# Kernel tuning notes

Measured on AMD Instinct MI355X. Metric: run time of the kernel, lower is better.

The kernel has to match this reference:

```python
import jax, jax.numpy as jnp
import numpy as np

D_MODEL = 1024
D_STATE = 16
BATCH = 2
SEQ = 2048


def setup_inputs() -> dict:
    key = jax.random.key(0)
    k1, k2, k3, k4, k5 = jax.random.split(key, 5)
    x = jax.random.normal(k1, (BATCH, SEQ, D_MODEL), dtype=jnp.float32)
    log_A_diag = jax.random.normal(k2, (D_MODEL, D_STATE), dtype=jnp.float32)
    B_w = jax.random.normal(k3, (D_STATE, D_MODEL), dtype=jnp.float32) / np.sqrt(D_MODEL)
    C_w = jax.random.normal(k4, (D_MODEL, D_STATE), dtype=jnp.float32) / np.sqrt(D_STATE)
    D_vec = jax.random.normal(k5, (D_MODEL,), dtype=jnp.float32)
    return {"x": x, "log_A_diag": log_A_diag, "B_w": B_w, "C_w": C_w, "D_vec": D_vec}


def reference(x, log_A_diag, B_w, C_w, D_vec):
    # x: (B, L, D)
    B, L, D = x.shape
    pad = 2 * L
    A_bar = jnp.exp(-jnp.exp(log_A_diag))          # (D, S), in (0, 1)
    B_t = jnp.einsum('bld,sd->bls', x, B_w)        # B projection: (B, L, S)
    k_idx = jnp.arange(L, dtype=x.dtype)
    kernel = A_bar[..., None] ** k_idx             # (D, S, L) exponential kernel
    # zero-padded FFT convolution along time axis
    kernel_fft = jnp.fft.rfft(kernel, n=pad, axis=-1)                 # (D, S, L+1)
    B_fft = jnp.fft.rfft(B_t.transpose(0, 2, 1), n=pad, axis=-1)      # (B, S, L+1)
    conv_fft = kernel_fft[None] * B_fft[:, None]                      # (B, D, S, L+1)
    conv = jnp.fft.irfft(conv_fft, n=pad, axis=-1)[..., :L]           # (B, D, S, L)
    # C projection fused over state dim; equivalent to permute->einsum('blds,ds->bld')
    y = jnp.einsum('bdsl,ds->bld', conv, C_w)
    y = y + D_vec[None, None, :] * x               # skip connection
    return y  # dropout is identity in eval mode
```

## Files before the change

### kernel.cpp

```cpp
#include <hip/hip_runtime.h>

#define D_MODEL 1024
#define D_STATE 16
#define BATCH   2
#define SEQ     2048
#define CHUNK   32
#define NCHUNK  (SEQ / CHUNK)
#define NGRP    (SEQ / 4)
#define Q       8
#define SBLEN   (SEQ / Q)
#define SBGRP   (SBLEN / 4)
#define SBCHK   (SBLEN / CHUNK)

__global__ __launch_bounds__(256) void k_bt(const float* __restrict__ x,
                                            const float* __restrict__ Bw,
                                            float* __restrict__ bt,
                                            float* __restrict__ btg) {
    const int t    = threadIdx.x;
    const int wave = t >> 6;
    const int lane = t & 63;

    float4 bw[4][4];
    const float* bwp = Bw + (wave * 4) * D_MODEL + lane * 16;
#pragma unroll
    for (int i = 0; i < 4; ++i)
#pragma unroll
        for (int k = 0; k < 4; ++k)
            bw[i][k] = *(const float4*)(bwp + i * D_MODEL + k * 4);

    const int ROWS = (BATCH * SEQ) / gridDim.x;
    const int row0 = blockIdx.x * ROWS;
    for (int r = 0; r < ROWS; ++r) {
        const int row = row0 + r;
        const float* xr = x + (size_t)row * D_MODEL + lane * 16;
        float4 xv[4];
#pragma unroll
        for (int k = 0; k < 4; ++k) xv[k] = *(const float4*)(xr + k * 4);

        float acc[4] = {0.f, 0.f, 0.f, 0.f};
#pragma unroll
        for (int i = 0; i < 4; ++i) {
#pragma unroll
            for (int k = 0; k < 4; ++k) {
                acc[i] += xv[k].x * bw[i][k].x;
                acc[i] += xv[k].y * bw[i][k].y;
                acc[i] += xv[k].z * bw[i][k].z;
                acc[i] += xv[k].w * bw[i][k].w;
            }
        }
#pragma unroll
        for (int m = 1; m < 64; m <<= 1) {
#pragma unroll
            for (int i = 0; i < 4; ++i) acc[i] += __shfl_xor(acc[i], m, 64);
        }
        if (lane == 0) {
            *(float4*)(bt + (size_t)row * D_STATE + wave * 4) =
                make_float4(acc[0], acc[1], acc[2], acc[3]);
            const int b = row >> 11;
            const int l = row & (SEQ - 1);
            float* p = btg + (((size_t)(b * NGRP + (l >> 2)) * D_STATE + wave * 4) << 2) + (l & 3);
#pragma unroll
            for (int i = 0; i < 4; ++i) p[i * 4] = acc[i];
        }
    }
}

__global__ __launch_bounds__(256) void k_scan_local(const float* __restrict__ btg,
                                                    const float* __restrict__ logA,
                                                    float* __restrict__ carry,
                                                    float* __restrict__ F) {
    const int blk = blockIdx.x;
    const int dt  = blk & 63;
    const int q   = (blk >> 6) & 7;
    const int b   = blk >> 9;
    const int t   = threadIdx.x;
    const int s   = t & 15;
    const int dl  = t >> 4;
    const int d   = dt * 16 + dl;

    __shared__ float sb[SBLEN * D_STATE];
    {
        const float4* src = (const float4*)(btg + (size_t)(b * NGRP + q * SBGRP) * (D_STATE * 4));
        float4* dst = (float4*)sb;
#pragma unroll
        for (int i = 0; i < 4; ++i) dst[t + i * 256] = src[t + i * 256];
    }
    __syncthreads();

    const float A  = expf(-expf(logA[d * D_STATE + s]));
    const float A2 = A * A, A4 = A2 * A2;

    const float4* sb4 = (const float4*)sb;
    float h = 0.f;
    size_t ci = ((size_t)(b * NCHUNK + q * SBCHK) * D_MODEL + d) * D_STATE + s;
#pragma unroll
    for (int k = 0; k < SBCHK; ++k) {
        carry[ci] = h;
        ci += (size_t)D_MODEL * D_STATE;
#pragma unroll
        for (int gg = 0; gg < CHUNK / 4; ++gg) {
            const float4 v = sb4[(k * (CHUNK / 4) + gg) * D_STATE + s];
            h = h * A4 + (((v.x * A + v.y) * A + v.z) * A + v.w);
        }
    }
    F[((size_t)(b * Q + q) * D_MODEL + d) * D_STATE + s] = h;
}

__global__ __launch_bounds__(256) void k_final(const float* __restrict__ x,
                                               const float* __restrict__ logA,
                                               const float* __restrict__ Cw,
                                               const float* __restrict__ Dv,
                                               const float* __restrict__ bt,
                                               const float* __restrict__ carry,
                                               const float* __restrict__ F,
                                               float* __restrict__ y) {
    const int blk = blockIdx.x;
    const int dt  = blk & 3;
    const int c   = (blk >> 2) & (NCHUNK - 1);
    const int b   = blk >> 8;
    const int t   = threadIdx.x;
    const int d   = dt * 256 + t;
    const int q   = c >> 3;
    const int kk  = c & 7;

    float A[D_STATE], C[D_STATE], h[D_STATE];
    const float* lp = logA + (size_t)d * D_STATE;
    const float* cp = Cw + (size_t)d * D_STATE;
    const float* hp = carry + ((size_t)(b * NCHUNK + c) * D_MODEL + d) * D_STATE;
#pragma unroll
    for (int s = 0; s < D_STATE; ++s) {
        A[s] = expf(-expf(lp[s]));
        C[s] = cp[s];
        h[s] = hp[s];
    }

    if (q > 0) {
        float A32[D_STATE], H[D_STATE];
#pragma unroll
        for (int s = 0; s < D_STATE; ++s) {
            float a = A[s];
            a *= a; a *= a; a *= a; a *= a; a *= a;
            A32[s] = a;
            H[s] = 0.f;
        }
        for (int p = 0; p < q; ++p) {
            const float* fp = F + ((size_t)(b * Q + p) * D_MODEL + d) * D_STATE;
#pragma unroll
            for (int s = 0; s < D_STATE; ++s) {
                float a256 = A32[s]; a256 *= a256; a256 *= a256; a256 *= a256;
                H[s] = H[s] * a256 + fp[s];
            }
        }
        for (int i = 0; i < kk; ++i)
#pragma unroll
            for (int s = 0; s < D_STATE; ++s) H[s] *= A32[s];
#pragma unroll
        for (int s = 0; s < D_STATE; ++s) h[s] += H[s];
    }

    const float dv = Dv[d];
    const float* btrow = bt + (size_t)(b * SEQ + c * CHUNK) * D_STATE;
    const size_t rowbase = (size_t)(b * SEQ + c * CHUNK) * D_MODEL + d;
    const float* xp = x + rowbase;
    float*       yp = y + rowbase;

#pragma unroll 4
    for (int j = 0; j < CHUNK; ++j) {
        float acc = dv * xp[(size_t)j * D_MODEL];
#pragma unroll
        for (int s = 0; s < D_STATE; ++s) {
            h[s] = A[s] * h[s] + btrow[j * D_STATE + s];
            acc += C[s] * h[s];
        }
        yp[(size_t)j * D_MODEL] = acc;
    }
}

extern "C" void kernel_launch(void* const* d_in, const int* in_sizes, int n_in,
                              void* d_out, int out_size, void* d_ws, size_t ws_size,
                              hipStream_t stream) {
    const float* x    = (const float*)d_in[0];
    const float* logA = (const float*)d_in[1];
    const float* Bw   = (const float*)d_in[2];
    const float* Cw   = (const float*)d_in[3];
    const float* Dv   = (const float*)d_in[4];
    float* y = (float*)d_out;

    float* bt    = (float*)d_ws;
    float* btg   = bt    + (size_t)BATCH * SEQ * D_STATE;
    float* carry = btg   + (size_t)BATCH * SEQ * D_STATE;
    float* F     = carry + (size_t)BATCH * NCHUNK * D_MODEL * D_STATE;

    hipLaunchKernelGGL(k_bt,         dim3(512), dim3(256), 0, stream, x, Bw, bt, btg);
    hipLaunchKernelGGL(k_scan_local, dim3(BATCH * Q * 64), dim3(256), 0, stream, btg, logA, carry, F);
    hipLaunchKernelGGL(k_final,      dim3(BATCH * NCHUNK * (D_MODEL / 256)), dim3(256), 0, stream, x, logA, Cw, Dv, bt, carry, F, y);
}
```

Baseline: 100.1 us.

## Fuse three kernels into one cooperative kernel with grid-wide syncs

Merges the B-projection, local chunk scan, and final output kernels into a single cooperative launch of 512 blocks, with grid syncs between phases replacing kernel boundaries. The scan phase now runs two work units per block so the grid stays at 512. This removes two kernel launch gaps and their inter-kernel drain and fill. In exchange it adds grid-barrier cost, and the combined kernel's register and LDS footprint could limit occupancy.

```diff
diff --git a/kernel.cpp b/kernel.cpp
--- a/kernel.cpp
+++ b/kernel.cpp
@@ -1,4 +1,7 @@
 #include <hip/hip_runtime.h>
+#include <hip/hip_cooperative_groups.h>
+
+namespace cg = cooperative_groups;
 
 #define D_MODEL 1024
 #define D_STATE 16
@@ -11,168 +14,172 @@
 #define SBLEN   (SEQ / Q)
 #define SBGRP   (SBLEN / 4)
 #define SBCHK   (SBLEN / CHUNK)
-
-__global__ __launch_bounds__(256) void k_bt(const float* __restrict__ x,
-                                            const float* __restrict__ Bw,
-                                            float* __restrict__ bt,
-                                            float* __restrict__ btg) {
-    const int t    = threadIdx.x;
-    const int wave = t >> 6;
-    const int lane = t & 63;
-
-    float4 bw[4][4];
-    const float* bwp = Bw + (wave * 4) * D_MODEL + lane * 16;
-#pragma unroll
-    for (int i = 0; i < 4; ++i)
-#pragma unroll
-        for (int k = 0; k < 4; ++k)
-            bw[i][k] = *(const float4*)(bwp + i * D_MODEL + k * 4);
-
-    const int ROWS = (BATCH * SEQ) / gridDim.x;
-    const int row0 = blockIdx.x * ROWS;
-    for (int r = 0; r < ROWS; ++r) {
-        const int row = row0 + r;
-        const float* xr = x + (size_t)row * D_MODEL + lane * 16;
-        float4 xv[4];
-#pragma unroll
-        for (int k = 0; k < 4; ++k) xv[k] = *(const float4*)(xr + k * 4);
-
-        float acc[4] = {0.f, 0.f, 0.f, 0.f};
-#pragma unroll
-        for (int i = 0; i < 4; ++i) {
-#pragma unroll
-            for (int k = 0; k < 4; ++k) {
-                acc[i] += xv[k].x * bw[i][k].x;
-                acc[i] += xv[k].y * bw[i][k].y;
-                acc[i] += xv[k].z * bw[i][k].z;
-                acc[i] += xv[k].w * bw[i][k].w;
-            }
-        }
-#pragma unroll
-        for (int m = 1; m < 64; m <<= 1) {
-#pragma unroll
-            for (int i = 0; i < 4; ++i) acc[i] += __shfl_xor(acc[i], m, 64);
-        }
-        if (lane == 0) {
-            *(float4*)(bt + (size_t)row * D_STATE + wave * 4) =
-                make_float4(acc[0], acc[1], acc[2], acc[3]);
-            const int b = row >> 11;
-            const int l = row & (SEQ - 1);
-            float* p = btg + (((size_t)(b * NGRP + (l >> 2)) * D_STATE + wave * 4) << 2) + (l & 3);
-#pragma unroll
-            for (int i = 0; i < 4; ++i) p[i * 4] = acc[i];
+#define GRID    512
+
+__global__ __launch_bounds__(256) void k_all(const float* __restrict__ x,
+                                             const float* __restrict__ logA,
+                                             const float* __restrict__ Bw,
+                                             const float* __restrict__ Cw,
+                                             const float* __restrict__ Dv,
+                                             float* __restrict__ bt,
+                                             float* __restrict__ btg,
+                                             float* __restrict__ carry,
+                                             float* __restrict__ F,
+                                             float* __restrict__ y) {
+    const int t = threadIdx.x;
+    __shared__ float sb[SBLEN * D_STATE];
+
+    {
+        const int wave = t >> 6;
+        const int lane = t & 63;
+
+        float4 bw[4][4];
+        const float* bwp = Bw + (wave * 4) * D_MODEL + lane * 16;
+#pragma unroll
+        for (int i = 0; i < 4; ++i)
+#pragma unroll
+            for (int k = 0; k < 4; ++k)
+                bw[i][k] = *(const float4*)(bwp + i * D_MODEL + k * 4);
+
+        const int ROWS = (BATCH * SEQ) / GRID;
+        const int row0 = blockIdx.x * ROWS;
+        for (int r = 0; r < ROWS; ++r) {
+            const int row = row0 + r;
+            const float* xr = x + (size_t)row * D_MODEL + lane * 16;
+            float4 xv[4];
+#pragma unroll
+            for (int k = 0; k < 4; ++k) xv[k] = *(const float4*)(xr + k * 4);
+
+            float acc[4] = {0.f, 0.f, 0.f, 0.f};
+#pragma unroll
+            for (int i = 0; i < 4; ++i) {
+#pragma unroll
+                for (int k = 0; k < 4; ++k) {
+                    acc[i] += xv[k].x * bw[i][k].x;
+                    acc[i] += xv[k].y * bw[i][k].y;
+                    acc[i] += xv[k].z * bw[i][k].z;
+                    acc[i] += xv[k].w * bw[i][k].w;
+                }
+            }
+#pragma unroll
+            for (int m = 1; m < 64; m <<= 1) {
+#pragma unroll
+                for (int i = 0; i < 4; ++i) acc[i] += __shfl_xor(acc[i], m, 64);
+            }
+            if (lane == 0) {
+                *(float4*)(bt + (size_t)row * D_STATE + wave * 4) =
+                    make_float4(acc[0], acc[1], acc[2], acc[3]);
+                const int b = row >> 11;
+                const int l = row & (SEQ - 1);
+                float* p = btg + (((size_t)(b * NGRP + (l >> 2)) * D_STATE + wave * 4) << 2) + (l & 3);
+#pragma unroll
+                for (int i = 0; i < 4; ++i) p[i * 4] = acc[i];
+            }
         }
     }
-}
-
-__global__ __launch_bounds__(256) void k_scan_local(const float* __restrict__ btg,
-                                                    const float* __restrict__ logA,
-                                                    float* __restrict__ carry,
-                                                    float* __restrict__ F) {
-    const int blk = blockIdx.x;
-    const int dt  = blk & 63;
-    const int q   = (blk >> 6) & 7;
-    const int b   = blk >> 9;
-    const int t   = threadIdx.x;
-    const int s   = t & 15;
-    const int dl  = t >> 4;
-    const int d   = dt * 16 + dl;
-
-    __shared__ float sb[SBLEN * D_STATE];
+
+    cg::this_grid().sync();
+
+#pragma unroll
+    for (int it = 0; it < 2; ++it) {
+        const int unit = blockIdx.x + it * GRID;
+        const int dt  = unit & 63;
+        const int q   = (unit >> 6) & 7;
+        const int b   = unit >> 9;
+        const int s   = t & 15;
+        const int dl  = t >> 4;
+        const int d   = dt * 16 + dl;
+
+        if (it) __syncthreads();
+        {
+            const float4* src = (const float4*)(btg + (size_t)(b * NGRP + q * SBGRP) * (D_STATE * 4));
+            float4* dst = (float4*)sb;
+#pragma unroll
+            for (int i = 0; i < 4; ++i) dst[t + i * 256] = src[t + i * 256];
+        }
+        __syncthreads();
+
+        const float A  = expf(-expf(logA[d * D_STATE + s]));
+        const float A2 = A * A, A4 = A2 * A2;
+
+        const float4* sb4 = (const float4*)sb;
+        float h = 0.f;
+        size_t ci = ((size_t)(b * NCHUNK + q * SBCHK) * D_MODEL + d) * D_STATE + s;
+#pragma unroll
+        for (int k = 0; k < SBCHK; ++k) {
+            carry[ci] = h;
+            ci += (size_t)D_MODEL * D_STATE;
+#pragma unroll
+            for (int gg = 0; gg < CHUNK / 4; ++gg) {
+                const float4 v = sb4[(k * (CHUNK / 4) + gg) * D_STATE + s];
+                h = h * A4 + (((v.x * A + v.y) * A + v.z) * A + v.w);
+            }
+        }
+        F[((size_t)(b * Q + q) * D_MODEL + d) * D_STATE + s] = h;
+    }
+
+    cg::this_grid().sync();
+
     {
-        const float4* src = (const float4*)(btg + (size_t)(b * NGRP + q * SBGRP) * (D_STATE * 4));
-        float4* dst = (float4*)sb;
-#pragma unroll
-        for (int i = 0; i < 4; ++i) dst[t + i * 256] = src[t + i * 256];
-    }
-    __syncthreads();
-
-    const float A  = expf(-expf(logA[d * D_STATE + s]));
-    const float A2 = A * A, A4 = A2 * A2;
-
-    const float4* sb4 = (const float4*)sb;
-    float h = 0.f;
-    size_t ci = ((size_t)(b * NCHUNK + q * SBCHK) * D_MODEL + d) * D_STATE + s;
-#pragma unroll
-    for (int k = 0; k < SBCHK; ++k) {
-        carry[ci] = h;
-        ci += (size_t)D_MODEL * D_STATE;
-#pragma unroll
-        for (int gg = 0; gg < CHUNK / 4; ++gg) {
-            const float4 v = sb4[(k * (CHUNK / 4) + gg) * D_STATE + s];
-            h = h * A4 + (((v.x * A + v.y) * A + v.z) * A + v.w);
-        }
-    }
-    F[((size_t)(b * Q + q) * D_MODEL + d) * D_STATE + s] = h;
-}
-
-__global__ __launch_bounds__(256) void k_final(const float* __restrict__ x,
-                                               const float* __restrict__ logA,
-                                               const float* __restrict__ Cw,
-                                               const float* __restrict__ Dv,
-                                               const float* __restrict__ bt,
-                                               const float* __restrict__ carry,
-                                               const float* __restrict__ F,
-                                               float* __restrict__ y) {
-    const int blk = blockIdx.x;
-    const int dt  = blk & 3;
-    const int c   = (blk >> 2) & (NCHUNK - 1);
-    const int b   = blk >> 8;
-    const int t   = threadIdx.x;
-    const int d   = dt * 256 + t;
-    const int q   = c >> 3;
-    const int kk  = c & 7;
-
-    float A[D_STATE], C[D_STATE], h[D_STATE];
-    const float* lp = logA + (size_t)d * D_STATE;
-    const float* cp = Cw + (size_t)d * D_STATE;
-    const float* hp = carry + ((size_t)(b * NCHUNK + c) * D_MODEL + d) * D_STATE;
-#pragma unroll
-    for (int s = 0; s < D_STATE; ++s) {
-        A[s] = expf(-expf(lp[s]));
-        C[s] = cp[s];
-        h[s] = hp[s];
-    }
-
-    if (q > 0) {
-        float A32[D_STATE], H[D_STATE];
+        const int blk = blockIdx.x;
+        const int dt  = blk & 3;
+        const int c   = (blk >> 2) & (NCHUNK - 1);
+        const int b   = blk >> 8;
+        const int d   = dt * 256 + t;
+        const int q   = c >> 3;
+        const int kk  = c & 7;
+
+        float A[D_STATE], C[D_STATE], h[D_STATE];
+        const float* lp = logA + (size_t)d * D_STATE;
+        const float* cp = Cw + (size_t)d * D_STATE;
+        const float* hp = carry + ((size_t)(b * NCHUNK + c) * D_MODEL + d) * D_STATE;
 #pragma unroll
         for (int s = 0; s < D_STATE; ++s) {
-            float a = A[s];
-            a *= a; a *= a; a *= a; a *= a; a *= a;
-            A32[s] = a;
-            H[s] = 0.f;
-        }
-        for (int p = 0; p < q; ++p) {
-            const float* fp = F + ((size_t)(b * Q + p) * D_MODEL + d) * D_STATE;
+            A[s] = expf(-expf(lp[s]));
+            C[s] = cp[s];
+            h[s] = hp[s];
+        }
+
+        if (q > 0) {
+            float A32[D_STATE], H[D_STATE];
 #pragma unroll
             for (int s = 0; s < D_STATE; ++s) {
-                float a256 = A32[s]; a256 *= a256; a256 *= a256; a256 *= a256;
-                H[s] = H[s] * a256 + fp[s];
-            }
-        }
-        for (int i = 0; i < kk; ++i)
-#pragma unroll
-            for (int s = 0; s < D_STATE; ++s) H[s] *= A32[s];
-#pragma unroll
-        for (int s = 0; s < D_STATE; ++s) h[s] += H[s];
-    }
-
-    const float dv = Dv[d];
-    const float* btrow = bt + (size_t)(b * SEQ + c * CHUNK) * D_STATE;
-    const size_t rowbase = (size_t)(b * SEQ + c * CHUNK) * D_MODEL + d;
-    const float* xp = x + rowbase;
-    float*       yp = y + rowbase;
+                float a = A[s];
+                a *= a; a *= a; a *= a; a *= a; a *= a;
+                A32[s] = a;
+                H[s] = 0.f;
+            }
+            for (int p = 0; p < q; ++p) {
+                const float* fp = F + ((size_t)(b * Q + p) * D_MODEL + d) * D_STATE;
+#pragma unroll
+                for (int s = 0; s < D_STATE; ++s) {
+                    float a256 = A32[s]; a256 *= a256; a256 *= a256; a256 *= a256;
+                    H[s] = H[s] * a256 + fp[s];
+                }
+            }
+            for (int i = 0; i < kk; ++i)
+#pragma unroll
+                for (int s = 0; s < D_STATE; ++s) H[s] *= A32[s];
+#pragma unroll
+            for (int s = 0; s < D_STATE; ++s) h[s] += H[s];
+        }
+
+        const float dv = Dv[d];
+        const float* btrow = bt + (size_t)(b * SEQ + c * CHUNK) * D_STATE;
+        const size_t rowbase = (size_t)(b * SEQ + c * CHUNK) * D_MODEL + d;
+        const float* xp = x + rowbase;
+        float*       yp = y + rowbase;
 
 #pragma unroll 4
-    for (int j = 0; j < CHUNK; ++j) {
-        float acc = dv * xp[(size_t)j * D_MODEL];
-#pragma unroll
-        for (int s = 0; s < D_STATE; ++s) {
-            h[s] = A[s] * h[s] + btrow[j * D_STATE + s];
-            acc += C[s] * h[s];
-        }
-        yp[(size_t)j * D_MODEL] = acc;
+        for (int j = 0; j < CHUNK; ++j) {
+            float acc = dv * xp[(size_t)j * D_MODEL];
+#pragma unroll
+            for (int s = 0; s < D_STATE; ++s) {
+                h[s] = A[s] * h[s] + btrow[j * D_STATE + s];
+                acc += C[s] * h[s];
+            }
+            yp[(size_t)j * D_MODEL] = acc;
+        }
     }
 }
 
@@ -191,7 +198,8 @@
     float* carry = btg   + (size_t)BATCH * SEQ * D_STATE;
     float* F     = carry + (size_t)BATCH * NCHUNK * D_MODEL * D_STATE;
 
-    hipLaunchKernelGGL(k_bt,         dim3(512), dim3(256), 0, stream, x, Bw, bt, btg);
-    hipLaunchKernelGGL(k_scan_local, dim3(BATCH * Q * 64), dim3(256), 0, stream, btg, logA, carry, F);
-    hipLaunchKernelGGL(k_final,      dim3(BATCH * NCHUNK * (D_MODEL / 256)), dim3(256), 0, stream, x, logA, Cw, Dv, bt, carry, F, y);
+    void* args[] = {(void*)&x, (void*)&logA, (void*)&Bw, (void*)&Cw, (void*)&Dv,
+                    (void*)&bt, (void*)&btg, (void*)&carry, (void*)&F, (void*)&y};
+    hipLaunchCooperativeKernel((const void*)k_all, dim3(GRID), dim3(256),
+                               args, 0, stream);
 }
```

Result: slower. 219.4 us (+119.0%).
